# Optimization experiments

Hardware: AMD Instinct MI355X
Metric: run time of the kernel (lower is better)

## Reference

```python
import jax, jax.numpy as jnp
import numpy as np

N = 50000
E = 625000
D = 128  # num_node_features == hidden_channels


def setup_inputs() -> dict:
    key = jax.random.key(0)
    ks = jax.random.split(key, 8)
    scale = 1.0 / np.sqrt(D)
    x = jax.random.normal(ks[0], (N, D), dtype=jnp.float32)
    edge_index = jax.random.randint(ks[1], (2, E), 0, N, dtype=jnp.int64)
    # PyG GraphConv params per layer: lin_rel (weight+bias) applied to aggregated
    # neighbors, lin_root (weight, no bias) applied to the node itself.
    W1_rel = jax.random.uniform(ks[2], (D, D), jnp.float32, -scale, scale)
    b1_rel = jnp.zeros((D,), jnp.float32)
    W1_root = jax.random.uniform(ks[3], (D, D), jnp.float32, -scale, scale)
    W2_rel = jax.random.uniform(ks[4], (D, D), jnp.float32, -scale, scale)
    b2_rel = jnp.zeros((D,), jnp.float32)
    W2_root = jax.random.uniform(ks[5], (D, D), jnp.float32, -scale, scale)
    return {"x": x, "edge_index": edge_index,
            "W1_rel": W1_rel, "b1_rel": b1_rel, "W1_root": W1_root,
            "W2_rel": W2_rel, "b2_rel": b2_rel, "W2_root": W2_root}


def reference(x, edge_index, W1_rel, b1_rel, W1_root, W2_rel, b2_rel, W2_root):
    src = edge_index[0]
    dst = edge_index[1]
    n = x.shape[0]

    def graph_conv(h, W_rel, b_rel, W_root):
        # aggregate-add neighbor features (gather by src, scatter-add at dst),
        # then linear on aggregate + linear on root node (PyG GraphConv).
        agg = jax.ops.segment_sum(h[src], dst, num_segments=n)  # [N, D]
        return agg @ W_rel + b_rel + h @ W_root

    h = jax.nn.relu(graph_conv(x, W1_rel, b1_rel, W1_root))
    # Dropout is identity in eval mode.
    h = graph_conv(h, W2_rel, b2_rel, W2_root)
    return h
```

## Files before the change

kernel.cpp:

```cpp
#include <hip/hip_runtime.h>

constexpr int D = 128;
constexpr int SCAN_CHUNK = 1024;

using short8 = __attribute__((ext_vector_type(8))) short;
using f32x4  = __attribute__((ext_vector_type(4))) float;

__device__ inline unsigned short f2bf(float f) {
    union { float f; unsigned u; } un;
    un.f = f;
    unsigned u = un.u;
    return (unsigned short)((u + 0x7fffu + ((u >> 16) & 1u)) >> 16);
}

__global__ void hist_kernel(const int* __restrict__ dst, int* __restrict__ deg,
                            int E) {
    int i = blockIdx.x * blockDim.x + threadIdx.x;
    if (i < E) atomicAdd(&deg[dst[i]], 1);
}

__global__ void block_reduce_kernel(const int* __restrict__ deg,
                                    int* __restrict__ bsums, int n) {
    __shared__ int wsum[4];
    const int t = threadIdx.x;
    const int lane = t & 63, w = t >> 6;
    int base = blockIdx.x * SCAN_CHUNK + t * 4;
    int s = 0;
#pragma unroll
    for (int j = 0; j < 4; ++j)
        if (base + j < n) s += deg[base + j];
#pragma unroll
    for (int off = 32; off > 0; off >>= 1) s += __shfl_down(s, off, 64);
    if (lane == 0) wsum[w] = s;
    __syncthreads();
    if (t == 0) bsums[blockIdx.x] = wsum[0] + wsum[1] + wsum[2] + wsum[3];
}

__global__ void scan_bsums_kernel(int* __restrict__ bsums, int nb,
                                  int* __restrict__ offs, int n) {
    const int t = threadIdx.x;
    int carry = 0;
    for (int base = 0; base < nb; base += 64) {
        int i = base + t;
        int v = (i < nb) ? bsums[i] : 0;
        int incl = v;
#pragma unroll
        for (int off = 1; off < 64; off <<= 1) {
            int u = __shfl_up(incl, off, 64);
            if (t >= off) incl += u;
        }
        if (i < nb) bsums[i] = incl - v + carry;
        carry += __shfl(incl, 63, 64);
    }
    if (t == 0) offs[n] = carry;
}

__global__ void scan_apply_kernel(const int* __restrict__ bsums,
                                  int* __restrict__ deg_cursor,
                                  int* __restrict__ offs, int n) {
    __shared__ int wsum[4];
    const int t = threadIdx.x;
    const int lane = t & 63, w = t >> 6;
    const int base = blockIdx.x * SCAN_CHUNK + t * 4;
    int v[4];
#pragma unroll
    for (int j = 0; j < 4; ++j)
        v[j] = (base + j < n) ? deg_cursor[base + j] : 0;
    int s = v[0] + v[1] + v[2] + v[3];
    int incl = s;
#pragma unroll
    for (int off = 1; off < 64; off <<= 1) {
        int u = __shfl_up(incl, off, 64);
        if (lane >= off) incl += u;
    }
    if (lane == 63) wsum[w] = incl;
    __syncthreads();
    int woff = 0;
    for (int i = 0; i < w; ++i) woff += wsum[i];
    int excl = incl - s + woff + bsums[blockIdx.x];
#pragma unroll
    for (int j = 0; j < 4; ++j) {
        if (base + j < n) {
            offs[base + j] = excl;
            deg_cursor[base + j] = excl;
        }
        excl += v[j];
    }
}

__global__ void reorder_kernel(const int* __restrict__ src,
                               const int* __restrict__ dst,
                               int* __restrict__ cursor,
                               int* __restrict__ esrc, int E) {
    int i = blockIdx.x * blockDim.x + threadIdx.x;
    if (i < E) {
        int d = dst[i];
        int p = atomicAdd(&cursor[d], 1);
        esrc[p] = src[i];
    }
}

__global__ void f32_to_bf16_kernel(const float* __restrict__ in,
                                   unsigned short* __restrict__ out,
                                   int nelem) {
    int i = (blockIdx.x * blockDim.x + threadIdx.x) * 4;
    if (i >= nelem) return;
    float4 v = *reinterpret_cast<const float4*>(in + i);
    unsigned short o[4];
    o[0] = f2bf(v.x); o[1] = f2bf(v.y); o[2] = f2bf(v.z); o[3] = f2bf(v.w);
    *reinterpret_cast<uint2*>(out + i) = *reinterpret_cast<uint2*>(o);
}

__global__ void build_bswz_kernel(const float* __restrict__ Wrel,
                                  const float* __restrict__ Wroot,
                                  unsigned short* __restrict__ bswz) {
    int idx = blockIdx.x * blockDim.x + threadIdx.x;
    if (idx >= 8 * 8 * 64) return;
    int lane = idx & 63;
    int t = (idx >> 6) & 7;
    int qq = idx >> 9;
    int col = t * 16 + (lane & 15);
    const float* W = (qq < 4) ? Wrel : Wroot;
    int kbase = (qq & 3) * 32 + ((lane >> 4) * 8);
    unsigned short o[8];
#pragma unroll
    for (int j = 0; j < 8; ++j) o[j] = f2bf(W[(size_t)(kbase + j) * D + col]);
    *reinterpret_cast<uint4*>(bswz + (size_t)idx * 8) =
        *reinterpret_cast<uint4*>(o);
}

__device__ inline void add8(float* acc, uint4 v) {
    const unsigned u0 = v.x, u1 = v.y, u2 = v.z, u3 = v.w;
    acc[0] += __uint_as_float(u0 << 16);
    acc[1] += __uint_as_float(u0 & 0xffff0000u);
    acc[2] += __uint_as_float(u1 << 16);
    acc[3] += __uint_as_float(u1 & 0xffff0000u);
    acc[4] += __uint_as_float(u2 << 16);
    acc[5] += __uint_as_float(u2 & 0xffff0000u);
    acc[6] += __uint_as_float(u3 << 16);
    acc[7] += __uint_as_float(u3 & 0xffff0000u);
}

__global__ void gather_bf16_kernel(const unsigned short* __restrict__ xb,
                                   const int* __restrict__ offs,
                                   const int* __restrict__ esrc,
                                   unsigned short* __restrict__ aggb, int n) {
    int tid = blockIdx.x * blockDim.x + threadIdx.x;
    int g = tid >> 4;
    int lane = tid & 15;
    if (g >= n) return;
    int beg = offs[g], end = offs[g + 1];
    float acc[8] = {0.f, 0.f, 0.f, 0.f, 0.f, 0.f, 0.f, 0.f};
    int j = beg;
    for (; j + 3 < end; j += 4) {
        int s0 = esrc[j], s1 = esrc[j + 1], s2 = esrc[j + 2], s3 = esrc[j + 3];
        uint4 v0 = *reinterpret_cast<const uint4*>(xb + (size_t)s0 * D + lane * 8);
        uint4 v1 = *reinterpret_cast<const uint4*>(xb + (size_t)s1 * D + lane * 8);
        uint4 v2 = *reinterpret_cast<const uint4*>(xb + (size_t)s2 * D + lane * 8);
        uint4 v3 = *reinterpret_cast<const uint4*>(xb + (size_t)s3 * D + lane * 8);
        add8(acc, v0); add8(acc, v1); add8(acc, v2); add8(acc, v3);
    }
    for (; j < end; ++j) {
        int s = esrc[j];
        uint4 v = *reinterpret_cast<const uint4*>(xb + (size_t)s * D + lane * 8);
        add8(acc, v);
    }
    unsigned short o[8];
#pragma unroll
    for (int i = 0; i < 8; ++i) o[i] = f2bf(acc[i]);
    *reinterpret_cast<uint4*>(aggb + (size_t)g * D + lane * 8) =
        *reinterpret_cast<uint4*>(o);
}

template <bool RELU, bool OUT_BF16>
__global__ __launch_bounds__(256) void mfma_gemm_kernel(
    const unsigned short* __restrict__ Ab, const unsigned short* __restrict__ Xb,
    const unsigned short* __restrict__ Bswz, const float* __restrict__ bias,
    unsigned short* __restrict__ outb, float* __restrict__ outf, int n) {
    const int t = threadIdx.x;
    const int lane = t & 63;
    const int w = t >> 6;
    const int quad = lane >> 4;
    const int l15 = lane & 15;
    const int R0 = blockIdx.x * 128 + w * 32;

    f32x4 acc[2][8];
#pragma unroll
    for (int rt = 0; rt < 2; ++rt)
#pragma unroll
        for (int nt = 0; nt < 8; ++nt)
            acc[rt][nt] = f32x4{0.f, 0.f, 0.f, 0.f};

    int rowA0 = R0 + l15;
    int rowA1 = R0 + 16 + l15;
    rowA0 = (rowA0 < n) ? rowA0 : (n - 1);
    rowA1 = (rowA1 < n) ? rowA1 : (n - 1);

    for (int qq = 0; qq < 8; ++qq) {
        const unsigned short* Asrc = (qq < 4) ? Ab : Xb;
        const int kb = (qq & 3) * 32 + quad * 8;
        short8 a0 = *reinterpret_cast<const short8*>(Asrc + (size_t)rowA0 * D + kb);
        short8 a1 = *reinterpret_cast<const short8*>(Asrc + (size_t)rowA1 * D + kb);
        const unsigned short* bp = Bswz + ((size_t)(qq * 8) * 64 + lane) * 8;
#pragma unroll
        for (int nt = 0; nt < 8; ++nt) {
            short8 b = *reinterpret_cast<const short8*>(bp + (size_t)nt * 64 * 8);
            acc[0][nt] = __builtin_amdgcn_mfma_f32_16x16x32_bf16(a0, b, acc[0][nt], 0, 0, 0);
            acc[1][nt] = __builtin_amdgcn_mfma_f32_16x16x32_bf16(a1, b, acc[1][nt], 0, 0, 0);
        }
    }

#pragma unroll
    for (int nt = 0; nt < 8; ++nt) {
        const int col = nt * 16 + l15;
        const float bv = bias[col];
#pragma unroll
        for (int rt = 0; rt < 2; ++rt) {
#pragma unroll
            for (int i = 0; i < 4; ++i) {
                int row = R0 + rt * 16 + quad * 4 + i;
                if (row < n) {
                    float v = acc[rt][nt][i] + bv;
                    if (RELU) v = fmaxf(v, 0.f);
                    if (OUT_BF16) outb[(size_t)row * D + col] = f2bf(v);
                    else outf[(size_t)row * D + col] = v;
                }
            }
        }
    }
}

__global__ void scatter_add_kernel(const float* __restrict__ x,
                                   const int* __restrict__ src,
                                   const int* __restrict__ dst,
                                   float* __restrict__ agg, int E) {
    int tid = blockIdx.x * blockDim.x + threadIdx.x;
    int e = tid >> 5;
    int lane = tid & 31;
    if (e >= E) return;
    int s = src[e];
    int d = dst[e];
    const float4 v = *reinterpret_cast<const float4*>(x + (size_t)s * D + lane * 4);
    float* a = agg + (size_t)d * D + lane * 4;
    unsafeAtomicAdd(a + 0, v.x);
    unsafeAtomicAdd(a + 1, v.y);
    unsafeAtomicAdd(a + 2, v.z);
    unsafeAtomicAdd(a + 3, v.w);
}

template <bool RELU>
__global__ __launch_bounds__(256) void dual_gemm_kernel(
    const float* __restrict__ agg, const float* __restrict__ hin,
    const float* __restrict__ Wrel, const float* __restrict__ brel,
    const float* __restrict__ Wroot, float* __restrict__ out, int n) {
    __shared__ float sA[32][D];
    __shared__ float sX[32][D];
    const int row0 = blockIdx.x * 32;
    const int t = threadIdx.x;
    for (int i = t; i < 32 * (D / 4); i += 256) {
        int r = i >> 5;
        int c = (i & 31) << 2;
        int row = row0 + r;
        float4 za = {0.f, 0.f, 0.f, 0.f};
        float4 zx = {0.f, 0.f, 0.f, 0.f};
        if (row < n) {
            za = *reinterpret_cast<const float4*>(agg + (size_t)row * D + c);
            zx = *reinterpret_cast<const float4*>(hin + (size_t)row * D + c);
        }
        *reinterpret_cast<float4*>(&sA[r][c]) = za;
        *reinterpret_cast<float4*>(&sX[r][c]) = zx;
    }
    __syncthreads();
    const int c4 = (t & 31) << 2;
    const int r0 = (t >> 5) << 2;
    float acc[4][4];
#pragma unroll
    for (int j = 0; j < 4; ++j)
#pragma unroll
        for (int c = 0; c < 4; ++c) acc[j][c] = 0.f;
    for (int k = 0; k < D; ++k) {
        const float4 wr = *reinterpret_cast<const float4*>(Wrel + k * D + c4);
        const float4 wo = *reinterpret_cast<const float4*>(Wroot + k * D + c4);
#pragma unroll
        for (int j = 0; j < 4; ++j) {
            const float a = sA[r0 + j][k];
            const float xv = sX[r0 + j][k];
            acc[j][0] = fmaf(a, wr.x, acc[j][0]);
            acc[j][1] = fmaf(a, wr.y, acc[j][1]);
            acc[j][2] = fmaf(a, wr.z, acc[j][2]);
            acc[j][3] = fmaf(a, wr.w, acc[j][3]);
            acc[j][0] = fmaf(xv, wo.x, acc[j][0]);
            acc[j][1] = fmaf(xv, wo.y, acc[j][1]);
            acc[j][2] = fmaf(xv, wo.z, acc[j][2]);
            acc[j][3] = fmaf(xv, wo.w, acc[j][3]);
        }
    }
    const float4 b = *reinterpret_cast<const float4*>(brel + c4);
#pragma unroll
    for (int j = 0; j < 4; ++j) {
        int row = row0 + r0 + j;
        if (row < n) {
            float4 v;
            v.x = acc[j][0] + b.x;
            v.y = acc[j][1] + b.y;
            v.z = acc[j][2] + b.z;
            v.w = acc[j][3] + b.w;
            if (RELU) {
                v.x = fmaxf(v.x, 0.f); v.y = fmaxf(v.y, 0.f);
                v.z = fmaxf(v.z, 0.f); v.w = fmaxf(v.w, 0.f);
            }
            *reinterpret_cast<float4*>(out + (size_t)row * D + c4) = v;
        }
    }
}

extern "C" void kernel_launch(void* const* d_in, const int* in_sizes, int n_in,
                              void* d_out, int out_size, void* d_ws,
                              size_t ws_size, hipStream_t stream) {
    const float* x       = (const float*)d_in[0];
    const int*   eidx    = (const int*)d_in[1];
    const float* W1_rel  = (const float*)d_in[2];
    const float* b1_rel  = (const float*)d_in[3];
    const float* W1_root = (const float*)d_in[4];
    const float* W2_rel  = (const float*)d_in[5];
    const float* b2_rel  = (const float*)d_in[6];
    const float* W2_root = (const float*)d_in[7];

    const int n = in_sizes[0] / D;
    const int E = in_sizes[1] / 2;
    const int* src = eidx;
    const int* dst = eidx + E;

    const int nb = (n + SCAN_CHUNK - 1) / SCAN_CHUNK;
    const size_t feat = (size_t)n * D;

    const size_t need = feat * 2 * 3 + 65536 * 2 * 2 +
                        ((size_t)(n + 1) + n + E + nb) * sizeof(int);

    if (ws_size >= need) {
        unsigned short* xb    = (unsigned short*)d_ws;
        unsigned short* hb    = xb + feat;
        unsigned short* aggb  = hb + feat;
        unsigned short* bswz1 = aggb + feat;
        unsigned short* bswz2 = bswz1 + 8 * 8 * 64 * 8;
        int* offs   = (int*)(bswz2 + 8 * 8 * 64 * 8);
        int* cursor = offs + (n + 1);
        int* esrc   = cursor + n;
        int* bsums  = esrc + E;

        hipMemsetAsync(cursor, 0, (size_t)n * sizeof(int), stream);
        hist_kernel<<<(E + 255) / 256, 256, 0, stream>>>(dst, cursor, E);
        block_reduce_kernel<<<nb, 256, 0, stream>>>(cursor, bsums, n);
        scan_bsums_kernel<<<1, 64, 0, stream>>>(bsums, nb, offs, n);
        scan_apply_kernel<<<nb, 256, 0, stream>>>(bsums, cursor, offs, n);
        reorder_kernel<<<(E + 255) / 256, 256, 0, stream>>>(src, dst, cursor,
                                                            esrc, E);

        f32_to_bf16_kernel<<<((int)feat / 4 + 255) / 256, 256, 0, stream>>>(
            x, xb, (int)feat);
        build_bswz_kernel<<<16, 256, 0, stream>>>(W1_rel, W1_root, bswz1);
        build_bswz_kernel<<<16, 256, 0, stream>>>(W2_rel, W2_root, bswz2);

        const int gth_blocks = (n * 16 + 255) / 256;
        const int gemm_blocks = (n + 127) / 128;

        gather_bf16_kernel<<<gth_blocks, 256, 0, stream>>>(xb, offs, esrc,
                                                           aggb, n);
        mfma_gemm_kernel<true, true><<<gemm_blocks, 256, 0, stream>>>(
            aggb, xb, bswz1, b1_rel, hb, nullptr, n);
        gather_bf16_kernel<<<gth_blocks, 256, 0, stream>>>(hb, offs, esrc,
                                                           aggb, n);
        mfma_gemm_kernel<false, false><<<gemm_blocks, 256, 0, stream>>>(
            aggb, hb, bswz2, b2_rel, nullptr, (float*)d_out, n);
    } else {
        float* agg = (float*)d_ws;
        float* h   = (float*)d_out;
        const size_t agg_bytes = feat * sizeof(float);
        const int sc_blocks = (E * 32 + 255) / 256;
        const int gemm_blocks = (n + 31) / 32;

        hipMemsetAsync(agg, 0, agg_bytes, stream);
        scatter_add_kernel<<<sc_blocks, 256, 0, stream>>>(x, src, dst, agg, E);
        dual_gemm_kernel<true><<<gemm_blocks, 256, 0, stream>>>(
            agg, x, W1_rel, b1_rel, W1_root, h, n);

        hipMemsetAsync(agg, 0, agg_bytes, stream);
        scatter_add_kernel<<<sc_blocks, 256, 0, stream>>>(h, src, dst, agg, E);
        dual_gemm_kernel<false><<<gemm_blocks, 256, 0, stream>>>(
            agg, h, W2_rel, b2_rel, W2_root, (float*)d_out, n);
    }
}
```

Baseline: 249.5 us.

## Fuse CSC build and weight/feature prep into one cooperative kernel

Replaces the memset, histogram, three scan kernels, reorder, bf16 conversion and two weight-swizzle launches with a single cooperative kernel that uses grid-wide syncs between phases. The aim is to cut per-launch overhead and idle gaps between the many small preprocessing kernels. The cost is several grid.sync barriers, and the fixed 1024-block grid must be co-resident on the device or the cooperative launch fails. The gather kernel also gets a cosmetic hoist of the per-lane offset.

```diff
diff --git a/kernel.cpp b/kernel.cpp
--- a/kernel.cpp
+++ b/kernel.cpp
@@ -1,7 +1,10 @@
 #include <hip/hip_runtime.h>
+#include <hip/hip_cooperative_groups.h>
+
+namespace cg = cooperative_groups;
 
 constexpr int D = 128;
-constexpr int SCAN_CHUNK = 1024;
+constexpr int COOP_GRID = 1024;
 
 using short8 = __attribute__((ext_vector_type(8))) short;
 using f32x4  = __attribute__((ext_vector_type(4))) float;
@@ -13,120 +16,121 @@
     return (unsigned short)((u + 0x7fffu + ((u >> 16) & 1u)) >> 16);
 }
 
-__global__ void hist_kernel(const int* __restrict__ dst, int* __restrict__ deg,
-                            int E) {
-    int i = blockIdx.x * blockDim.x + threadIdx.x;
-    if (i < E) atomicAdd(&deg[dst[i]], 1);
-}
-
-__global__ void block_reduce_kernel(const int* __restrict__ deg,
-                                    int* __restrict__ bsums, int n) {
+__global__ __launch_bounds__(256) void prep_csc_kernel(
+    const float* __restrict__ x,
+    const float* __restrict__ W1_rel, const float* __restrict__ W1_root,
+    const float* __restrict__ W2_rel, const float* __restrict__ W2_root,
+    const int* __restrict__ src, const int* __restrict__ dst,
+    unsigned short* __restrict__ xb,
+    unsigned short* __restrict__ bswz1, unsigned short* __restrict__ bswz2,
+    int* __restrict__ deg_cursor, int* __restrict__ offs,
+    int* __restrict__ esrc, int* __restrict__ bsums,
+    int n, int E, int feat4, int nb) {
+    cg::grid_group grid = cg::this_grid();
     __shared__ int wsum[4];
-    const int t = threadIdx.x;
-    const int lane = t & 63, w = t >> 6;
-    int base = blockIdx.x * SCAN_CHUNK + t * 4;
-    int s = 0;
-#pragma unroll
-    for (int j = 0; j < 4; ++j)
-        if (base + j < n) s += deg[base + j];
-#pragma unroll
-    for (int off = 32; off > 0; off >>= 1) s += __shfl_down(s, off, 64);
-    if (lane == 0) wsum[w] = s;
-    __syncthreads();
-    if (t == 0) bsums[blockIdx.x] = wsum[0] + wsum[1] + wsum[2] + wsum[3];
-}
-
-__global__ void scan_bsums_kernel(int* __restrict__ bsums, int nb,
-                                  int* __restrict__ offs, int n) {
-    const int t = threadIdx.x;
-    int carry = 0;
-    for (int base = 0; base < nb; base += 64) {
-        int i = base + t;
-        int v = (i < nb) ? bsums[i] : 0;
-        int incl = v;
+    const int gtid = blockIdx.x * blockDim.x + threadIdx.x;
+    const int gsz = gridDim.x * blockDim.x;
+
+    for (int i = gtid; i < n; i += gsz) deg_cursor[i] = 0;
+    for (int i = gtid; i < feat4; i += gsz) {
+        float4 v = reinterpret_cast<const float4*>(x)[i];
+        unsigned short o[4] = {f2bf(v.x), f2bf(v.y), f2bf(v.z), f2bf(v.w)};
+        reinterpret_cast<uint2*>(xb)[i] = *reinterpret_cast<uint2*>(o);
+    }
+    for (int idx = gtid; idx < 2 * 4096; idx += gsz) {
+        const int which = idx >> 12;
+        const int id = idx & 4095;
+        const int lane = id & 63;
+        const int t = (id >> 6) & 7;
+        const int qq = id >> 9;
+        const float* W = (qq < 4) ? (which ? W2_rel : W1_rel)
+                                  : (which ? W2_root : W1_root);
+        const int col = t * 16 + (lane & 15);
+        const int kbase = (qq & 3) * 32 + ((lane >> 4) * 8);
+        unsigned short o[8];
+#pragma unroll
+        for (int j = 0; j < 8; ++j)
+            o[j] = f2bf(W[(size_t)(kbase + j) * D + col]);
+        uint4* dp = reinterpret_cast<uint4*>((which ? bswz2 : bswz1) +
+                                             (size_t)id * 8);
+        *dp = *reinterpret_cast<uint4*>(o);
+    }
+    grid.sync();
+
+    for (int i = gtid; i < E; i += gsz) atomicAdd(&deg_cursor[dst[i]], 1);
+    grid.sync();
+
+    if ((int)blockIdx.x < nb) {
+        const int t = threadIdx.x;
+        const int lane = t & 63, w = t >> 6;
+        const int base = blockIdx.x * 1024 + t * 4;
+        int s = 0;
+#pragma unroll
+        for (int j = 0; j < 4; ++j)
+            if (base + j < n) s += deg_cursor[base + j];
+#pragma unroll
+        for (int off = 32; off > 0; off >>= 1) s += __shfl_down(s, off, 64);
+        if (lane == 0) wsum[w] = s;
+        __syncthreads();
+        if (t == 0) bsums[blockIdx.x] = wsum[0] + wsum[1] + wsum[2] + wsum[3];
+    }
+    grid.sync();
+
+    if (blockIdx.x == 0 && threadIdx.x < 64) {
+        const int t = threadIdx.x;
+        int carry = 0;
+        for (int base = 0; base < nb; base += 64) {
+            const int i = base + t;
+            int v = (i < nb) ? bsums[i] : 0;
+            int incl = v;
+#pragma unroll
+            for (int off = 1; off < 64; off <<= 1) {
+                int u = __shfl_up(incl, off, 64);
+                if (t >= off) incl += u;
+            }
+            if (i < nb) bsums[i] = incl - v + carry;
+            carry += __shfl(incl, 63, 64);
+        }
+        if (t == 0) offs[n] = carry;
+    }
+    grid.sync();
+
+    if ((int)blockIdx.x < nb) {
+        const int t = threadIdx.x;
+        const int lane = t & 63, w = t >> 6;
+        const int base = blockIdx.x * 1024 + t * 4;
+        int v[4];
+#pragma unroll
+        for (int j = 0; j < 4; ++j)
+            v[j] = (base + j < n) ? deg_cursor[base + j] : 0;
+        const int s = v[0] + v[1] + v[2] + v[3];
+        int incl = s;
 #pragma unroll
         for (int off = 1; off < 64; off <<= 1) {
             int u = __shfl_up(incl, off, 64);
-            if (t >= off) incl += u;
-        }
-        if (i < nb) bsums[i] = incl - v + carry;
-        carry += __shfl(incl, 63, 64);
-    }
-    if (t == 0) offs[n] = carry;
-}
-
-__global__ void scan_apply_kernel(const int* __restrict__ bsums,
-                                  int* __restrict__ deg_cursor,
-                                  int* __restrict__ offs, int n) {
-    __shared__ int wsum[4];
-    const int t = threadIdx.x;
-    const int lane = t & 63, w = t >> 6;
-    const int base = blockIdx.x * SCAN_CHUNK + t * 4;
-    int v[4];
-#pragma unroll
-    for (int j = 0; j < 4; ++j)
-        v[j] = (base + j < n) ? deg_cursor[base + j] : 0;
-    int s = v[0] + v[1] + v[2] + v[3];
-    int incl = s;
-#pragma unroll
-    for (int off = 1; off < 64; off <<= 1) {
-        int u = __shfl_up(incl, off, 64);
-        if (lane >= off) incl += u;
-    }
-    if (lane == 63) wsum[w] = incl;
-    __syncthreads();
-    int woff = 0;
-    for (int i = 0; i < w; ++i) woff += wsum[i];
-    int excl = incl - s + woff + bsums[blockIdx.x];
-#pragma unroll
-    for (int j = 0; j < 4; ++j) {
-        if (base + j < n) {
-            offs[base + j] = excl;
-            deg_cursor[base + j] = excl;
-        }
-        excl += v[j];
-    }
-}
-
-__global__ void reorder_kernel(const int* __restrict__ src,
-                               const int* __restrict__ dst,
-                               int* __restrict__ cursor,
-                               int* __restrict__ esrc, int E) {
-    int i = blockIdx.x * blockDim.x + threadIdx.x;
-    if (i < E) {
-        int d = dst[i];
-        int p = atomicAdd(&cursor[d], 1);
+            if (lane >= off) incl += u;
+        }
+        if (lane == 63) wsum[w] = incl;
+        __syncthreads();
+        int woff = 0;
+        for (int i = 0; i < w; ++i) woff += wsum[i];
+        int excl = incl - s + woff + bsums[blockIdx.x];
+#pragma unroll
+        for (int j = 0; j < 4; ++j) {
+            if (base + j < n) {
+                offs[base + j] = excl;
+                deg_cursor[base + j] = excl;
+            }
+            excl += v[j];
+        }
+    }
+    grid.sync();
+
+    for (int i = gtid; i < E; i += gsz) {
+        const int d = dst[i];
+        const int p = atomicAdd(&deg_cursor[d], 1);
         esrc[p] = src[i];
     }
-}
-
-__global__ void f32_to_bf16_kernel(const float* __restrict__ in,
-                                   unsigned short* __restrict__ out,
-                                   int nelem) {
-    int i = (blockIdx.x * blockDim.x + threadIdx.x) * 4;
-    if (i >= nelem) return;
-    float4 v = *reinterpret_cast<const float4*>(in + i);
-    unsigned short o[4];
-    o[0] = f2bf(v.x); o[1] = f2bf(v.y); o[2] = f2bf(v.z); o[3] = f2bf(v.w);
-    *reinterpret_cast<uint2*>(out + i) = *reinterpret_cast<uint2*>(o);
-}
-
-__global__ void build_bswz_kernel(const float* __restrict__ Wrel,
-                                  const float* __restrict__ Wroot,
-                                  unsigned short* __restrict__ bswz) {
-    int idx = blockIdx.x * blockDim.x + threadIdx.x;
-    if (idx >= 8 * 8 * 64) return;
-    int lane = idx & 63;
-    int t = (idx >> 6) & 7;
-    int qq = idx >> 9;
-    int col = t * 16 + (lane & 15);
-    const float* W = (qq < 4) ? Wrel : Wroot;
-    int kbase = (qq & 3) * 32 + ((lane >> 4) * 8);
-    unsigned short o[8];
-#pragma unroll
-    for (int j = 0; j < 8; ++j) o[j] = f2bf(W[(size_t)(kbase + j) * D + col]);
-    *reinterpret_cast<uint4*>(bswz + (size_t)idx * 8) =
-        *reinterpret_cast<uint4*>(o);
 }
 
 __device__ inline void add8(float* acc, uint4 v) {
@@ -150,19 +154,19 @@
     int lane = tid & 15;
     if (g >= n) return;
     int beg = offs[g], end = offs[g + 1];
+    const size_t loff = (size_t)lane * 8;
     float acc[8] = {0.f, 0.f, 0.f, 0.f, 0.f, 0.f, 0.f, 0.f};
     int j = beg;
     for (; j + 3 < end; j += 4) {
         int s0 = esrc[j], s1 = esrc[j + 1], s2 = esrc[j + 2], s3 = esrc[j + 3];
-        uint4 v0 = *reinterpret_cast<const uint4*>(xb + (size_t)s0 * D + lane * 8);
-        uint4 v1 = *reinterpret_cast<const uint4*>(xb + (size_t)s1 * D + lane * 8);
-        uint4 v2 = *reinterpret_cast<const uint4*>(xb + (size_t)s2 * D + lane * 8);
-        uint4 v3 = *reinterpret_cast<const uint4*>(xb + (size_t)s3 * D + lane * 8);
+        uint4 v0 = *reinterpret_cast<const uint4*>(xb + (size_t)s0 * D + loff);
+        uint4 v1 = *reinterpret_cast<const uint4*>(xb + (size_t)s1 * D + loff);
+        uint4 v2 = *reinterpret_cast<const uint4*>(xb + (size_t)s2 * D + loff);
+        uint4 v3 = *reinterpret_cast<const uint4*>(xb + (size_t)s3 * D + loff);
         add8(acc, v0); add8(acc, v1); add8(acc, v2); add8(acc, v3);
     }
     for (; j < end; ++j) {
-        int s = esrc[j];
-        uint4 v = *reinterpret_cast<const uint4*>(xb + (size_t)s * D + lane * 8);
+        uint4 v = *reinterpret_cast<const uint4*>(xb + (size_t)esrc[j] * D + loff);
         add8(acc, v);
     }
     unsigned short o[8];
@@ -331,7 +335,7 @@
     const int* src = eidx;
     const int* dst = eidx + E;
 
-    const int nb = (n + SCAN_CHUNK - 1) / SCAN_CHUNK;
+    const int nb = (n + 1023) / 1024;
     const size_t feat = (size_t)n * D;
 
     const size_t need = feat * 2 * 3 + 65536 * 2 * 2 +
@@ -348,18 +352,17 @@
         int* esrc   = cursor + n;
         int* bsums  = esrc + E;
 
-        hipMemsetAsync(cursor, 0, (size_t)n * sizeof(int), stream);
-        hist_kernel<<<(E + 255) / 256, 256, 0, stream>>>(dst, cursor, E);
-        block_reduce_kernel<<<nb, 256, 0, stream>>>(cursor, bsums, n);
-        scan_bsums_kernel<<<1, 64, 0, stream>>>(bsums, nb, offs, n);
-        scan_apply_kernel<<<nb, 256, 0, stream>>>(bsums, cursor, offs, n);
-        reorder_kernel<<<(E + 255) / 256, 256, 0, stream>>>(src, dst, cursor,
-                                                            esrc, E);
-
-        f32_to_bf16_kernel<<<((int)feat / 4 + 255) / 256, 256, 0, stream>>>(
-            x, xb, (int)feat);
-        build_bswz_kernel<<<16, 256, 0, stream>>>(W1_rel, W1_root, bswz1);
-        build_bswz_kernel<<<16, 256, 0, stream>>>(W2_rel, W2_root, bswz2);
+        int n2 = n, E2 = E, feat4 = (int)(feat / 4), nbv = nb;
+        void* kargs[] = {
+            (void*)&x, (void*)&W1_rel, (void*)&W1_root,
+            (void*)&W2_rel, (void*)&W2_root,
+            (void*)&src, (void*)&dst,
+            (void*)&xb, (void*)&bswz1, (void*)&bswz2,
+            (void*)&cursor, (void*)&offs, (void*)&esrc, (void*)&bsums,
+            (void*)&n2, (void*)&E2, (void*)&feat4, (void*)&nbv};
+        hipLaunchCooperativeKernel((const void*)prep_csc_kernel,
+                                   dim3(COOP_GRID), dim3(256), kargs, 0,
+                                   stream);
 
         const int gth_blocks = (n * 16 + 255) / 256;
         const int gemm_blocks = (n + 127) / 128;
```

Result: slower. 761.9 us (+205.3%).
